# Optimization experiments

Hardware: AMD Instinct MI355X
Metric: run time of the kernel (lower is better)

Reference implementation:

```python
import jax, jax.numpy as jnp
import numpy as np

B_SZ, T, D_MODEL, N_STATE = 4, 4096, 1024, 256
D_FF = ((int(8 / 3 * D_MODEL) + 7) // 8) * 8  # 2736
EPS = 1e-6


def setup_inputs() -> dict:
    key = jax.random.key(0)
    ks = jax.random.split(key, 8)
    return {
        "x": jax.random.normal(ks[0], (B_SZ, T, D_MODEL), dtype=jnp.float32),
        "log_lambda": jax.random.normal(ks[1], (N_STATE,), dtype=jnp.float32) * 0.5 + 3.0,
        "B_w": jax.random.normal(ks[2], (N_STATE, D_MODEL), dtype=jnp.float32) / np.sqrt(D_MODEL),
        "C_w": jax.random.normal(ks[3], (D_MODEL, N_STATE), dtype=jnp.float32) / np.sqrt(N_STATE),
        "D_skip": jnp.zeros((D_MODEL,), dtype=jnp.float32),
        "ssm_norm_w": jnp.ones((D_MODEL,), dtype=jnp.float32),
        "ffn_norm_w": jnp.ones((D_MODEL,), dtype=jnp.float32),
        "w1": jax.random.normal(ks[4], (D_FF, D_MODEL), dtype=jnp.float32) / np.sqrt(D_MODEL),
        "w2": jax.random.normal(ks[5], (D_MODEL, D_FF), dtype=jnp.float32) / np.sqrt(D_FF),
        "w3": jax.random.normal(ks[6], (D_FF, D_MODEL), dtype=jnp.float32) / np.sqrt(D_MODEL),
    }


def _rmsnorm(x, w):
    rms = jnp.sqrt(jnp.mean(x * x, axis=-1, keepdims=True) + EPS)
    return x / rms * w


def reference(x, log_lambda, B_w, C_w, D_skip, ssm_norm_w, ffn_norm_w, w1, w2, w3):
    # --- SSM branch ---
    u = _rmsnorm(x, ssm_norm_w)                       # [B,T,D]
    lam = jax.nn.sigmoid(log_lambda)                  # [N]
    Bu = jnp.einsum("btd,nd->btn", u, B_w)            # [B,T,N]

    def step(h, bu_t):                                 # h: [B,N], bu_t: [B,N]
        h = lam * h + bu_t
        return h, h

    h0 = jnp.zeros((x.shape[0], log_lambda.shape[0]), dtype=x.dtype)
    _, hs = jax.lax.scan(step, h0, jnp.swapaxes(Bu, 0, 1))  # hs: [T,B,N]
    hs = jnp.swapaxes(hs, 0, 1)                        # [B,T,N]
    y = jnp.einsum("btn,dn->btd", hs, C_w) + D_skip * u
    x = x + y

    # --- FFN branch (SwiGLU) ---
    z = _rmsnorm(x, ffn_norm_w)
    gate = jax.nn.silu(jnp.einsum("btd,fd->btf", z, w1))
    val = jnp.einsum("btd,fd->btf", z, w3)
    ffn = jnp.einsum("btf,df->btd", gate * val, w2)
    return x + ffn
```

## Files before the change

### kernel.cpp

```cpp
#include <hip/hip_runtime.h>
#include <hip/hip_bf16.h>
#include <cstdint>

#define BSZ   4
#define TLEN  4096
#define DM    1024
#define NS    256
#define DFF   2736
#define DFFP  2816
#define NCHUNK 64
#define CLEN   64

typedef __attribute__((ext_vector_type(8))) short bf16x8;
typedef __attribute__((ext_vector_type(4))) float f32x4;

__device__ __forceinline__ float bf2f(ushort u) {
  union { unsigned int i; float f; } v; v.i = ((unsigned int)u) << 16; return v.f;
}
__device__ __forceinline__ ushort f2bf(float f) {
  union { float f; unsigned int i; } v; v.f = f;
  unsigned int r = v.i + 0x7FFFu + ((v.i >> 16) & 1u);
  return (ushort)(r >> 16);
}
__device__ __forceinline__ void gload16(const ushort* g, ushort* l) {
  __builtin_amdgcn_global_load_lds((const __attribute__((address_space(1))) void*)g,
                                   (__attribute__((address_space(3))) void*)l, 16, 0, 0);
}

__global__ void convert_pad(const float* __restrict__ src, ushort* __restrict__ dst,
                            int srcR, int srcC, int dstR, int dstC) {
  long total = (long)dstR * dstC / 4;
  for (long q = (long)blockIdx.x * blockDim.x + threadIdx.x; q < total;
       q += (long)gridDim.x * blockDim.x) {
    long e = q * 4;
    int r = (int)(e / dstC);
    int c = (int)(e % dstC);
    ushort4 o;
    float v0 = (r < srcR && c + 0 < srcC) ? src[(long)r * srcC + c + 0] : 0.f;
    float v1 = (r < srcR && c + 1 < srcC) ? src[(long)r * srcC + c + 1] : 0.f;
    float v2 = (r < srcR && c + 2 < srcC) ? src[(long)r * srcC + c + 2] : 0.f;
    float v3 = (r < srcR && c + 3 < srcC) ? src[(long)r * srcC + c + 3] : 0.f;
    o.x = f2bf(v0); o.y = f2bf(v1); o.z = f2bf(v2); o.w = f2bf(v3);
    *(ushort4*)(dst + e) = o;
  }
}

__global__ __launch_bounds__(256) void rmsnorm_bf16(const float* __restrict__ x,
                                                    const float* __restrict__ w,
                                                    ushort* __restrict__ out) {
  long row = blockIdx.x;
  int tid = threadIdx.x;
  const float4* xr = (const float4*)(x + row * DM);
  float4 v = xr[tid];
  float ss = v.x * v.x + v.y * v.y + v.z * v.z + v.w * v.w;
#pragma unroll
  for (int m = 32; m >= 1; m >>= 1) ss += __shfl_xor(ss, m);
  __shared__ float red[4];
  if ((tid & 63) == 0) red[tid >> 6] = ss;
  __syncthreads();
  float tot = red[0] + red[1] + red[2] + red[3];
  float inv = rsqrtf(tot * (1.0f / DM) + 1e-6f);
  float4 wv = ((const float4*)w)[tid];
  ushort4 o;
  o.x = f2bf(v.x * inv * wv.x);
  o.y = f2bf(v.y * inv * wv.y);
  o.z = f2bf(v.z * inv * wv.z);
  o.w = f2bf(v.w * inv * wv.w);
  ((ushort4*)(out + row * DM))[tid] = o;
}

__global__ __launch_bounds__(256) void scan_local(float* __restrict__ Bu,
                                                  float* __restrict__ E,
                                                  const float* __restrict__ loglam) {
  int bc = blockIdx.x;
  int b = bc / NCHUNK, c = bc % NCHUNK;
  int n = threadIdx.x;
  float lam = 1.f / (1.f + __expf(-loglam[n]));
  float h = 0.f;
  long base = ((long)b * TLEN + (long)c * CLEN) * NS + n;
#pragma unroll 4
  for (int t = 0; t < CLEN; ++t) {
    long idx = base + (long)t * NS;
    h = lam * h + Bu[idx];
    Bu[idx] = h;
  }
  E[((long)b * NCHUNK + c) * NS + n] = h;
}

__global__ __launch_bounds__(1024) void scan_carry(const float* __restrict__ E,
                                                   float* __restrict__ C,
                                                   const float* __restrict__ loglam) {
  int tid = threadIdx.x;
  int b = tid >> 8, n = tid & 255;
  float lam = 1.f / (1.f + __expf(-loglam[n]));
  float lamL = lam;
#pragma unroll
  for (int i = 0; i < 6; ++i) lamL *= lamL;
  float carry = 0.f;
  for (int c = 0; c < NCHUNK; ++c) {
    long idx = ((long)b * NCHUNK + c) * NS + n;
    C[idx] = carry;
    carry = lamL * carry + E[idx];
  }
}

__global__ __launch_bounds__(256) void scan_fix(const float* __restrict__ local,
                                                const float* __restrict__ Carry,
                                                const float* __restrict__ loglam,
                                                ushort* __restrict__ hsb) {
  int bc = blockIdx.x;
  int b = bc / NCHUNK, c = bc % NCHUNK;
  int n = threadIdx.x;
  float lam = 1.f / (1.f + __expf(-loglam[n]));
  float p = Carry[((long)b * NCHUNK + c) * NS + n];
  long base = ((long)b * TLEN + (long)c * CLEN) * NS + n;
#pragma unroll 4
  for (int t = 0; t < CLEN; ++t) {
    p *= lam;
    long idx = base + (long)t * NS;
    hsb[idx] = f2bf(local[idx] + p);
  }
}

template <int EPI>
__global__ __launch_bounds__(256, 2) void gemm_bt(
    const ushort* __restrict__ A, const ushort* __restrict__ B0, const ushort* __restrict__ B1,
    float* __restrict__ outF, ushort* __restrict__ outU,
    const float* __restrict__ xin, const float* __restrict__ dskip,
    const ushort* __restrict__ uin, int M, int N, int K) {
  constexpr bool DUAL = (EPI == 2);
  __shared__ ushort sA[128 * 32];
  __shared__ ushort sB[128 * 32];
  __shared__ ushort sB1[DUAL ? 128 * 32 : 4];

  int tid = threadIdx.x;
  int lane = tid & 63;
  int wid = tid >> 6;
  int nbx = N >> 7;
  int by = blockIdx.x / nbx;
  int bx = blockIdx.x - by * nbx;
  long brow = (long)by << 7;
  long bcol = (long)bx << 7;

  int srow = tid >> 2;
  int scol = (tid & 3) << 3;
  const ushort* gA = A + (brow + srow) * (long)K + scol;
  const ushort* gB = B0 + (bcol + srow) * (long)K + scol;
  const ushort* gB1p = nullptr;
  if constexpr (DUAL) gB1p = B1 + (bcol + srow) * (long)K + scol;
  ushort* lA = sA + (wid << 9);
  ushort* lB = sB + (wid << 9);
  ushort* lB1 = sB1 + (wid << 9);

  int wr = wid >> 1, wc = wid & 1;
  int fr = lane & 15;
  int fk = (lane >> 4) << 3;

  f32x4 acc0[4][4];
  f32x4 acc1[DUAL ? 4 : 1][DUAL ? 4 : 1];
#pragma unroll
  for (int i = 0; i < 4; ++i)
#pragma unroll
    for (int j = 0; j < 4; ++j) {
      acc0[i][j] = (f32x4)0.f;
      if constexpr (DUAL) acc1[i][j] = (f32x4)0.f;
    }

  long rowq = 64 * (long)K;
  for (int kt = 0; kt < K; kt += 32) {
    __syncthreads();
    gload16(gA + kt, lA);
    gload16(gA + kt + rowq, lA + 2048);
    gload16(gB + kt, lB);
    gload16(gB + kt + rowq, lB + 2048);
    if constexpr (DUAL) {
      gload16(gB1p + kt, lB1);
      gload16(gB1p + kt + rowq, lB1 + 2048);
    }
    __syncthreads();

    bf16x8 a[4], b[4], b2[4];
#pragma unroll
    for (int i = 0; i < 4; ++i)
      a[i] = *(const bf16x8*)(sA + ((wr * 64 + i * 16 + fr) * 32 + fk));
#pragma unroll
    for (int j = 0; j < 4; ++j) {
      b[j] = *(const bf16x8*)(sB + ((wc * 64 + j * 16 + fr) * 32 + fk));
      if constexpr (DUAL)
        b2[j] = *(const bf16x8*)(sB1 + ((wc * 64 + j * 16 + fr) * 32 + fk));
    }
#pragma unroll
    for (int i = 0; i < 4; ++i)
#pragma unroll
      for (int j = 0; j < 4; ++j) {
        acc0[i][j] = __builtin_amdgcn_mfma_f32_16x16x32_bf16(a[i], b[j], acc0[i][j], 0, 0, 0);
        if constexpr (DUAL)
          acc1[i][j] = __builtin_amdgcn_mfma_f32_16x16x32_bf16(a[i], b2[j], acc1[i][j], 0, 0, 0);
      }
  }

#pragma unroll
  for (int i = 0; i < 4; ++i) {
    int rowb = wr * 64 + i * 16 + ((lane >> 4) << 2);
#pragma unroll
    for (int j = 0; j < 4; ++j) {
      long gcol = bcol + wc * 64 + j * 16 + fr;
#pragma unroll
      for (int r = 0; r < 4; ++r) {
        long grow = brow + rowb + r;
        long idx = grow * N + gcol;
        float v = acc0[i][j][r];
        if constexpr (EPI == 0) {
          outF[idx] = v;
        } else if constexpr (EPI == 1) {
          outF[idx] = v + xin[idx] + dskip[gcol] * bf2f(uin[idx]);
        } else if constexpr (EPI == 2) {
          float s = v / (1.f + __expf(-v));
          outU[idx] = f2bf(s * acc1[i][j][r]);
        } else {
          outF[idx] += v;
        }
      }
    }
  }
}

extern "C" void kernel_launch(void* const* d_in, const int* in_sizes, int n_in,
                              void* d_out, int out_size, void* d_ws, size_t ws_size,
                              hipStream_t stream) {
  const float* x      = (const float*)d_in[0];
  const float* loglam = (const float*)d_in[1];
  const float* B_w    = (const float*)d_in[2];
  const float* C_w    = (const float*)d_in[3];
  const float* D_skip = (const float*)d_in[4];
  const float* ssm_w  = (const float*)d_in[5];
  const float* ffn_w  = (const float*)d_in[6];
  const float* w1     = (const float*)d_in[7];
  const float* w2     = (const float*)d_in[8];
  const float* w3     = (const float*)d_in[9];
  float* out = (float*)d_out;

  char* ws = (char*)d_ws;
  ushort* u_bf  = (ushort*)(ws + 0);
  float*  Bu    = (float*) (ws + 33554432);
  ushort* hs_bf = (ushort*)(ws + 50331648);
  float*  E     = (float*) (ws + 58720256);
  float*  Carry = (float*) (ws + 58982400);
  ushort* wB    = (ushort*)(ws + 59244544);
  ushort* wC    = (ushort*)(ws + 59768832);
  ushort* w1p   = (ushort*)(ws + 60293120);
  ushort* w3p   = (ushort*)(ws + 66060288);
  ushort* w2p   = (ushort*)(ws + 71827456);
  ushort* gv    = (ushort*)(ws + 77594624);

  auto cvb = [](long elems) {
    long q = elems / 4;
    long b = (q + 255) / 256;
    return (int)(b > 4096 ? 4096 : b);
  };

  convert_pad<<<cvb(256L * 1024), 256, 0, stream>>>(B_w, wB, 256, 1024, 256, 1024);
  convert_pad<<<cvb(1024L * 256), 256, 0, stream>>>(C_w, wC, 1024, 256, 1024, 256);
  convert_pad<<<cvb((long)DFFP * 1024), 256, 0, stream>>>(w1, w1p, DFF, 1024, DFFP, 1024);
  convert_pad<<<cvb((long)DFFP * 1024), 256, 0, stream>>>(w3, w3p, DFF, 1024, DFFP, 1024);
  convert_pad<<<cvb(1024L * DFFP), 256, 0, stream>>>(w2, w2p, 1024, DFF, 1024, DFFP);

  rmsnorm_bf16<<<BSZ * TLEN, 256, 0, stream>>>(x, ssm_w, u_bf);
  gemm_bt<0><<<(16384 / 128) * (NS / 128), 256, 0, stream>>>(
      u_bf, wB, nullptr, Bu, nullptr, nullptr, nullptr, nullptr, 16384, NS, DM);
  scan_local<<<BSZ * NCHUNK, 256, 0, stream>>>(Bu, E, loglam);
  scan_carry<<<1, 1024, 0, stream>>>(E, Carry, loglam);
  scan_fix<<<BSZ * NCHUNK, 256, 0, stream>>>(Bu, Carry, loglam, hs_bf);
  gemm_bt<1><<<(16384 / 128) * (DM / 128), 256, 0, stream>>>(
      hs_bf, wC, nullptr, out, nullptr, x, D_skip, u_bf, 16384, DM, NS);

  rmsnorm_bf16<<<BSZ * TLEN, 256, 0, stream>>>(out, ffn_w, u_bf);
  gemm_bt<2><<<(16384 / 128) * (DFFP / 128), 256, 0, stream>>>(
      u_bf, w1p, w3p, nullptr, gv, nullptr, nullptr, nullptr, 16384, DFFP, DM);
  gemm_bt<3><<<(16384 / 128) * (DM / 128), 256, 0, stream>>>(
      gv, w2p, nullptr, out, nullptr, nullptr, nullptr, nullptr, 16384, DM, DFFP);
}
```

Before: 650.2 us.

## Add pipelined 256x128 FFN GEMM with interleaved W1/W3 packing

Replaces the two FFN GEMMs with a new 512-thread kernel that uses 256x128 tiles, K-step 64, a triple-buffered LDS pipeline with async global-to-LDS loads, XOR swizzled LDS layout, and a grouped block order. W1 and W3 are packed into one interleaved matrix in 16-row groups, so a single GEMM produces gate and value columns side by side and the SwiGLU epilogue pairs adjacent tiles. The aim is to hide load latency, cut LDS bank conflicts and raise MFMA utilisation in the dominant GEMMs. In exchange it requests 144KB of dynamic LDS per block, which limits how many blocks fit per CU, and the per-call weight packing stays in the timed path.

```diff
diff --git a/kernel.cpp b/kernel.cpp
--- a/kernel.cpp
+++ b/kernel.cpp
@@ -8,6 +8,7 @@
 #define NS    256
 #define DFF   2736
 #define DFFP  2816
+#define NPK   5632
 #define NCHUNK 64
 #define CLEN   64
 
@@ -45,6 +46,27 @@
   }
 }
 
+__global__ void pack_w13(const float* __restrict__ w1, const float* __restrict__ w3,
+                         ushort* __restrict__ wp) {
+  long total = (long)NPK * DM / 4;
+  for (long q = (long)blockIdx.x * blockDim.x + threadIdx.x; q < total;
+       q += (long)gridDim.x * blockDim.x) {
+    long e = q * 4;
+    int r = (int)(e >> 10);
+    int c = (int)(e & 1023);
+    int f = ((r >> 5) << 4) + (r & 15);
+    const float* src = ((r >> 4) & 1) ? w3 : w1;
+    ushort4 o;
+    if (f < DFF) {
+      const float4 v = *(const float4*)(src + (long)f * DM + c);
+      o.x = f2bf(v.x); o.y = f2bf(v.y); o.z = f2bf(v.z); o.w = f2bf(v.w);
+    } else {
+      o.x = o.y = o.z = o.w = 0;
+    }
+    *(ushort4*)(wp + e) = o;
+  }
+}
+
 __global__ __launch_bounds__(256) void rmsnorm_bf16(const float* __restrict__ x,
                                                     const float* __restrict__ w,
                                                     ushort* __restrict__ out) {
@@ -124,14 +146,12 @@
 
 template <int EPI>
 __global__ __launch_bounds__(256, 2) void gemm_bt(
-    const ushort* __restrict__ A, const ushort* __restrict__ B0, const ushort* __restrict__ B1,
-    float* __restrict__ outF, ushort* __restrict__ outU,
+    const ushort* __restrict__ A, const ushort* __restrict__ B0,
+    float* __restrict__ outF,
     const float* __restrict__ xin, const float* __restrict__ dskip,
     const ushort* __restrict__ uin, int M, int N, int K) {
-  constexpr bool DUAL = (EPI == 2);
   __shared__ ushort sA[128 * 32];
   __shared__ ushort sB[128 * 32];
-  __shared__ ushort sB1[DUAL ? 128 * 32 : 4];
 
   int tid = threadIdx.x;
   int lane = tid & 63;
@@ -146,25 +166,18 @@
   int scol = (tid & 3) << 3;
   const ushort* gA = A + (brow + srow) * (long)K + scol;
   const ushort* gB = B0 + (bcol + srow) * (long)K + scol;
-  const ushort* gB1p = nullptr;
-  if constexpr (DUAL) gB1p = B1 + (bcol + srow) * (long)K + scol;
   ushort* lA = sA + (wid << 9);
   ushort* lB = sB + (wid << 9);
-  ushort* lB1 = sB1 + (wid << 9);
 
   int wr = wid >> 1, wc = wid & 1;
   int fr = lane & 15;
   int fk = (lane >> 4) << 3;
 
   f32x4 acc0[4][4];
-  f32x4 acc1[DUAL ? 4 : 1][DUAL ? 4 : 1];
 #pragma unroll
   for (int i = 0; i < 4; ++i)
 #pragma unroll
-    for (int j = 0; j < 4; ++j) {
-      acc0[i][j] = (f32x4)0.f;
-      if constexpr (DUAL) acc1[i][j] = (f32x4)0.f;
-    }
+    for (int j = 0; j < 4; ++j) acc0[i][j] = (f32x4)0.f;
 
   long rowq = 64 * (long)K;
   for (int kt = 0; kt < K; kt += 32) {
@@ -173,30 +186,20 @@
     gload16(gA + kt + rowq, lA + 2048);
     gload16(gB + kt, lB);
     gload16(gB + kt + rowq, lB + 2048);
-    if constexpr (DUAL) {
-      gload16(gB1p + kt, lB1);
-      gload16(gB1p + kt + rowq, lB1 + 2048);
-    }
     __syncthreads();
 
-    bf16x8 a[4], b[4], b2[4];
+    bf16x8 a[4], b[4];
 #pragma unroll
     for (int i = 0; i < 4; ++i)
       a[i] = *(const bf16x8*)(sA + ((wr * 64 + i * 16 + fr) * 32 + fk));
 #pragma unroll
-    for (int j = 0; j < 4; ++j) {
+    for (int j = 0; j < 4; ++j)
       b[j] = *(const bf16x8*)(sB + ((wc * 64 + j * 16 + fr) * 32 + fk));
-      if constexpr (DUAL)
-        b2[j] = *(const bf16x8*)(sB1 + ((wc * 64 + j * 16 + fr) * 32 + fk));
-    }
 #pragma unroll
     for (int i = 0; i < 4; ++i)
 #pragma unroll
-      for (int j = 0; j < 4; ++j) {
+      for (int j = 0; j < 4; ++j)
         acc0[i][j] = __builtin_amdgcn_mfma_f32_16x16x32_bf16(a[i], b[j], acc0[i][j], 0, 0, 0);
-        if constexpr (DUAL)
-          acc1[i][j] = __builtin_amdgcn_mfma_f32_16x16x32_bf16(a[i], b2[j], acc1[i][j], 0, 0, 0);
-      }
   }
 
 #pragma unroll
@@ -212,13 +215,181 @@
         float v = acc0[i][j][r];
         if constexpr (EPI == 0) {
           outF[idx] = v;
-        } else if constexpr (EPI == 1) {
+        } else {
           outF[idx] = v + xin[idx] + dskip[gcol] * bf2f(uin[idx]);
-        } else if constexpr (EPI == 2) {
-          float s = v / (1.f + __expf(-v));
-          outU[idx] = f2bf(s * acc1[i][j][r]);
-        } else {
-          outF[idx] += v;
+        }
+      }
+    }
+  }
+}
+
+template <bool DUAL>
+__global__ __launch_bounds__(512, 2) void big_gemm(
+    const ushort* __restrict__ A, const ushort* __restrict__ Bm,
+    float* __restrict__ outF, ushort* __restrict__ outU) {
+  constexpr int K = DUAL ? DM : DFFP;
+  constexpr int N = DUAL ? NPK : DM;
+  constexpr int NT = K / 64;
+  constexpr int NBX = N / 128;
+  constexpr int NWG = 64 * NBX;
+  constexpr int BUFE = 24576;
+  extern __shared__ __align__(16) char smem_raw[];
+  ushort* lds = (ushort*)smem_raw;
+
+  int tid = threadIdx.x;
+  int lane = tid & 63;
+  int wid = tid >> 6;
+
+  int bid = blockIdx.x;
+  int swz = (bid & 7) * (NWG >> 3) + (bid >> 3);
+  int by = swz & 63;
+  int bx = swz >> 6;
+  long brow = (long)by << 8;
+  long bcol = (long)bx << 7;
+
+  uint aOff[4]; int aDst[4];
+  uint bOff[2]; int bDst[2];
+#pragma unroll
+  for (int q = 0; q < 4; ++q) {
+    int slot = q * 512 + tid;
+    int row = slot >> 3, cs = slot & 7;
+    int csx = cs ^ (row & 7);
+    aOff[q] = (uint)((brow + row) * (long)K + csx * 8);
+    aDst[q] = q * 4096 + wid * 512;
+  }
+#pragma unroll
+  for (int q = 0; q < 2; ++q) {
+    int slot = q * 512 + tid;
+    int row = slot >> 3, cs = slot & 7;
+    int csx = cs ^ (row & 7);
+    bOff[q] = (uint)((bcol + row) * (long)K + csx * 8);
+    bDst[q] = 16384 + q * 4096 + wid * 512;
+  }
+
+  int wrm = wid >> 1, wcn = wid & 1;
+  int fr = lane & 15, fq = lane >> 4;
+  int aAdr[2][4], bAdr[2][4];
+#pragma unroll
+  for (int kk = 0; kk < 2; ++kk)
+#pragma unroll
+    for (int i = 0; i < 4; ++i) {
+      int row = wrm * 64 + i * 16 + fr;
+      aAdr[kk][i] = row * 64 + (((kk * 4 + fq) ^ (row & 7)) << 3);
+      int rowb = wcn * 64 + i * 16 + fr;
+      bAdr[kk][i] = 16384 + rowb * 64 + (((kk * 4 + fq) ^ (rowb & 7)) << 3);
+    }
+
+  auto STAGE = [&](int g, int buf) {
+    const ushort* Ag = A + (long)g * 64;
+    const ushort* Bg = Bm + (long)g * 64;
+    ushort* lb = lds + buf * BUFE;
+#pragma unroll
+    for (int q = 0; q < 4; ++q) gload16(Ag + aOff[q], lb + aDst[q]);
+#pragma unroll
+    for (int q = 0; q < 2; ++q) gload16(Bg + bOff[q], lb + bDst[q]);
+  };
+
+  f32x4 acc[4][4];
+#pragma unroll
+  for (int i = 0; i < 4; ++i)
+#pragma unroll
+    for (int j = 0; j < 4; ++j) acc[i][j] = (f32x4)0.f;
+
+  STAGE(0, 0);
+  STAGE(1, 1);
+  asm volatile("s_waitcnt vmcnt(6)" ::: "memory");
+  asm volatile("s_barrier" ::: "memory");
+
+  int cb = 0, sb = 2;
+#pragma unroll 1
+  for (int g = 0; g < NT - 2; ++g) {
+    const ushort* lb = lds + cb * BUFE;
+    bf16x8 a[2][4], b[2][4];
+#pragma unroll
+    for (int kk = 0; kk < 2; ++kk)
+#pragma unroll
+      for (int i = 0; i < 4; ++i) {
+        a[kk][i] = *(const bf16x8*)(lb + aAdr[kk][i]);
+        b[kk][i] = *(const bf16x8*)(lb + bAdr[kk][i]);
+      }
+    STAGE(g + 2, sb);
+#pragma unroll
+    for (int kk = 0; kk < 2; ++kk)
+#pragma unroll
+      for (int i = 0; i < 4; ++i)
+#pragma unroll
+        for (int j = 0; j < 4; ++j)
+          acc[i][j] = __builtin_amdgcn_mfma_f32_16x16x32_bf16(a[kk][i], b[kk][j], acc[i][j], 0, 0, 0);
+    asm volatile("s_waitcnt vmcnt(6)" ::: "memory");
+    asm volatile("s_barrier" ::: "memory");
+    cb = (cb == 2) ? 0 : cb + 1;
+    sb = (sb == 2) ? 0 : sb + 1;
+  }
+  {
+    const ushort* lb = lds + cb * BUFE;
+    bf16x8 a[2][4], b[2][4];
+#pragma unroll
+    for (int kk = 0; kk < 2; ++kk)
+#pragma unroll
+      for (int i = 0; i < 4; ++i) {
+        a[kk][i] = *(const bf16x8*)(lb + aAdr[kk][i]);
+        b[kk][i] = *(const bf16x8*)(lb + bAdr[kk][i]);
+      }
+#pragma unroll
+    for (int kk = 0; kk < 2; ++kk)
+#pragma unroll
+      for (int i = 0; i < 4; ++i)
+#pragma unroll
+        for (int j = 0; j < 4; ++j)
+          acc[i][j] = __builtin_amdgcn_mfma_f32_16x16x32_bf16(a[kk][i], b[kk][j], acc[i][j], 0, 0, 0);
+    asm volatile("s_waitcnt vmcnt(0)" ::: "memory");
+    asm volatile("s_barrier" ::: "memory");
+    cb = (cb == 2) ? 0 : cb + 1;
+  }
+  {
+    const ushort* lb = lds + cb * BUFE;
+    bf16x8 a[2][4], b[2][4];
+#pragma unroll
+    for (int kk = 0; kk < 2; ++kk)
+#pragma unroll
+      for (int i = 0; i < 4; ++i) {
+        a[kk][i] = *(const bf16x8*)(lb + aAdr[kk][i]);
+        b[kk][i] = *(const bf16x8*)(lb + bAdr[kk][i]);
+      }
+#pragma unroll
+    for (int kk = 0; kk < 2; ++kk)
+#pragma unroll
+      for (int i = 0; i < 4; ++i)
+#pragma unroll
+        for (int j = 0; j < 4; ++j)
+          acc[i][j] = __builtin_amdgcn_mfma_f32_16x16x32_bf16(a[kk][i], b[kk][j], acc[i][j], 0, 0, 0);
+  }
+
+#pragma unroll
+  for (int i = 0; i < 4; ++i) {
+    int rowb = wrm * 64 + i * 16 + fq * 4;
+    if constexpr (DUAL) {
+#pragma unroll
+      for (int jp = 0; jp < 2; ++jp) {
+        int j = jp * 2;
+        long fcol = (bcol >> 1) + wcn * 32 + jp * 16 + fr;
+#pragma unroll
+        for (int r = 0; r < 4; ++r) {
+          long grow = brow + rowb + r;
+          float gt = acc[i][j][r];
+          float vl = acc[i][j + 1][r];
+          float s = gt / (1.f + __expf(-gt));
+          outU[grow * DFFP + fcol] = f2bf(s * vl);
+        }
+      }
+    } else {
+#pragma unroll
+      for (int j = 0; j < 4; ++j) {
+        long gcol = bcol + wcn * 64 + j * 16 + fr;
+#pragma unroll
+        for (int r = 0; r < 4; ++r) {
+          long grow = brow + rowb + r;
+          outF[grow * DM + gcol] += acc[i][j][r];
         }
       }
     }
@@ -248,10 +419,15 @@
   float*  Carry = (float*) (ws + 58982400);
   ushort* wB    = (ushort*)(ws + 59244544);
   ushort* wC    = (ushort*)(ws + 59768832);
-  ushort* w1p   = (ushort*)(ws + 60293120);
-  ushort* w3p   = (ushort*)(ws + 66060288);
+  ushort* Wp    = (ushort*)(ws + 60293120);
   ushort* w2p   = (ushort*)(ws + 71827456);
   ushort* gv    = (ushort*)(ws + 77594624);
+
+  constexpr int BIG_LDS = 147456;
+  (void)hipFuncSetAttribute((const void*)&big_gemm<true>,
+                            hipFuncAttributeMaxDynamicSharedMemorySize, BIG_LDS);
+  (void)hipFuncSetAttribute((const void*)&big_gemm<false>,
+                            hipFuncAttributeMaxDynamicSharedMemorySize, BIG_LDS);
 
   auto cvb = [](long elems) {
     long q = elems / 4;
@@ -261,22 +437,19 @@
 
   convert_pad<<<cvb(256L * 1024), 256, 0, stream>>>(B_w, wB, 256, 1024, 256, 1024);
   convert_pad<<<cvb(1024L * 256), 256, 0, stream>>>(C_w, wC, 1024, 256, 1024, 256);
-  convert_pad<<<cvb((long)DFFP * 1024), 256, 0, stream>>>(w1, w1p, DFF, 1024, DFFP, 1024);
-  convert_pad<<<cvb((long)DFFP * 1024), 256, 0, stream>>>(w3, w3p, DFF, 1024, DFFP, 1024);
+  pack_w13<<<2048, 256, 0, stream>>>(w1, w3, Wp);
   convert_pad<<<cvb(1024L * DFFP), 256, 0, stream>>>(w2, w2p, 1024, DFF, 1024, DFFP);
 
   rmsnorm_bf16<<<BSZ * TLEN, 256, 0, stream>>>(x, ssm_w, u_bf);
   gemm_bt<0><<<(16384 / 128) * (NS / 128), 256, 0, stream>>>(
-      u_bf, wB, nullptr, Bu, nullptr, nullptr, nullptr, nullptr, 16384, NS, DM);
+      u_bf, wB, Bu, nullptr, nullptr, nullptr, 16384, NS, DM);
   scan_local<<<BSZ * NCHUNK, 256, 0, stream>>>(Bu, E, loglam);
   scan_carry<<<1, 1024, 0, stream>>>(E, Carry, loglam);
   scan_fix<<<BSZ * NCHUNK, 256, 0, stream>>>(Bu, Carry, loglam, hs_bf);
   gemm_bt<1><<<(16384 / 128) * (DM / 128), 256, 0, stream>>>(
-      hs_bf, wC, nullptr, out, nullptr, x, D_skip, u_bf, 16384, DM, NS);
+      hs_bf, wC, out, x, D_skip, u_bf, 16384, DM, NS);
 
   rmsnorm_bf16<<<BSZ * TLEN, 256, 0, stream>>>(out, ffn_w, u_bf);
-  gemm_bt<2><<<(16384 / 128) * (DFFP / 128), 256, 0, stream>>>(
-      u_bf, w1p, w3p, nullptr, gv, nullptr, nullptr, nullptr, 16384, DFFP, DM);
-  gemm_bt<3><<<(16384 / 128) * (DM / 128), 256, 0, stream>>>(
-      gv, w2p, nullptr, out, nullptr, nullptr, nullptr, nullptr, 16384, DM, DFFP);
-}
+  big_gemm<true><<<64 * (NPK / 128), 512, BIG_LDS, stream>>>(u_bf, Wp, nullptr, gv);
+  big_gemm<false><<<64 * (DM / 128), 512, BIG_LDS, stream>>>(gv, w2p, out, nullptr);
+}
```

After: 622.6 us. -4.2%, faster.
